# Kernel tuning notes

Hardware: AMD Instinct MI355X
Metric: run time of the kernel (lower is better)

Reference implementation:

```python
import jax, jax.numpy as jnp
import numpy as np

B, T, TREF, NBINS, H = 4096, 8192, 8192, 50, 32  # np.linspace(lo,hi,50) -> 49 bins
EPS = 1e-10


def setup_inputs() -> dict:
    key = jax.random.key(0)
    k0, k1, k2, k3, k4, k5 = jax.random.split(key, 6)
    return {
        "current_returns": jax.random.normal(k0, (B, T), jnp.float32) * 0.02,
        "reference_returns": jax.random.normal(k1, (TREF,), jnp.float32) * 0.02,
        "w1": jax.random.normal(k2, (H, 1), jnp.float32) * 0.5,   # Linear(1, H).weight
        "b1": jax.random.normal(k3, (H,), jnp.float32) * 0.1,
        "w2": jax.random.normal(k4, (H, H), jnp.float32) * 0.1,   # Linear(H, H).weight
        "b2": jax.random.normal(k5, (H,), jnp.float32) * 0.1,
    }


def _kl_from_hists(ref, curr, ref_min, ref_max):
    # Faithful to InformationTheory.kl_divergence with n_bins=50 (49 equal-width bins).
    nb = NBINS - 1
    lo = jnp.minimum(ref_min, curr.min())
    hi = jnp.maximum(ref_max, curr.max())
    width = (hi - lo) / nb

    def hist_density(x):
        # np.histogram(x, bins=linspace(lo,hi,50), density=True); all x in [lo,hi],
        # right edge goes to last bin (handled by clip).
        idx = jnp.clip(jnp.floor((x - lo) / width).astype(jnp.int32), 0, nb - 1)
        counts = jnp.zeros(nb, jnp.float32).at[idx].add(1.0)
        return counts / (x.shape[0] * width)

    p = hist_density(ref) + EPS
    q = hist_density(curr) + EPS
    p = p / p.sum()
    q = q / q.sum()
    return jnp.sum(p * jnp.log(p / q))


def reference(current_returns, reference_returns, w1, b1, w2, b2):
    ref = reference_returns
    ref_min, ref_max = ref.min(), ref.max()
    kl = jax.vmap(lambda c: _kl_from_hists(ref, c, ref_min, ref_max))(current_returns)  # [B]
    kl = jax.lax.stop_gradient(kl)  # original detaches before building kl_tensor
    x = kl[:, None]                                  # [B, 1]
    h = jax.nn.relu(x @ w1.T + b1)                   # [B, H]
    encoded = h @ w2.T + b2                          # [B, H]
    return kl, encoded
```

## Files before the change

kernel.cpp:

```cpp
#include <hip/hip_runtime.h>
#include <math.h>

constexpr int T_LEN  = 8192;
constexpr int B_ROWS = 4096;
constexpr int NB     = 49;
constexpr int NC     = 32;
constexpr int HDIM   = 32;
constexpr int FBINS  = 8192;
constexpr int ROWS   = 4;
constexpr float EPSF = 1e-10f;

constexpr int WS_CDF_OFF    = 8;
constexpr int WS_BINNED_OFF = 8208;

#define HP(i) ((i) + ((i) >> 5))

__device__ __forceinline__ void sync_lds() {
    asm volatile("s_waitcnt lgkmcnt(0)" ::: "memory");
    __builtin_amdgcn_s_barrier();
    __builtin_amdgcn_sched_barrier(0);
}

__global__ __launch_bounds__(256)
void ref_cdf_kernel(const float* __restrict__ ref, float* __restrict__ wsf) {
    __shared__ float sv[FBINS];
    __shared__ int   hist[HP(FBINS)];
    __shared__ int   wsum[4];
    __shared__ float rmn4[4], rmx4[4];
    const int tid  = threadIdx.x;
    const int lane = tid & 63;
    const int wave = tid >> 6;

    const float4* r4 = (const float4*)ref;
    float4* sv4 = (float4*)sv;
    float mn = 3.0e38f, mx = -3.0e38f;
    #pragma unroll
    for (int i = 0; i < 8; ++i) {
        float4 v = r4[tid + i * 256];
        sv4[tid + i * 256] = v;
        mn = fminf(mn, fminf(fminf(v.x, v.y), fminf(v.z, v.w)));
        mx = fmaxf(mx, fmaxf(fmaxf(v.x, v.y), fmaxf(v.z, v.w)));
    }
    for (int i = tid; i < HP(FBINS); i += 256) hist[i] = 0;
    #pragma unroll
    for (int off = 32; off > 0; off >>= 1) {
        mn = fminf(mn, __shfl_xor(mn, off));
        mx = fmaxf(mx, __shfl_xor(mx, off));
    }
    if (lane == 0) { rmn4[wave] = mn; rmx4[wave] = mx; }
    __syncthreads();
    const float rmin = fminf(fminf(rmn4[0], rmn4[1]), fminf(rmn4[2], rmn4[3]));
    const float rmax = fmaxf(fmaxf(rmx4[0], rmx4[1]), fmaxf(rmx4[2], rmx4[3]));
    const float finv = (float)FBINS / (rmax - rmin);

    for (int i = tid; i < FBINS; i += 256) {
        int fb = min(max((int)((sv[i] - rmin) * finv), 0), FBINS - 1);
        atomicAdd(&hist[HP(fb)], 1);
    }
    __syncthreads();

    const int base = tid * 32;
    int s = 0;
    #pragma unroll
    for (int j = 0; j < 32; ++j) {
        int h = hist[HP(base + j)]; hist[HP(base + j)] = s; s += h;
    }
    const int own = s;
    int incl = s;
    #pragma unroll
    for (int off = 1; off < 64; off <<= 1) {
        int t = __shfl_up(incl, off);
        if (lane >= off) incl += t;
    }
    if (lane == 63) wsum[wave] = incl;
    __syncthreads();
    int woff = 0;
    #pragma unroll
    for (int w = 0; w < 4; ++w) if (w < wave) woff += wsum[w];
    const int add = woff + incl - own;
    #pragma unroll
    for (int j = 0; j < 32; ++j) hist[HP(base + j)] += add;
    __syncthreads();

    int* cdf = (int*)(wsf + WS_CDF_OFF);
    for (int i = tid; i < FBINS; i += 256) cdf[i] = hist[HP(i)];
    if (tid == 0) { cdf[FBINS] = T_LEN; wsf[0] = rmin; wsf[1] = rmax; }
    __syncthreads();

    float* binned = wsf + WS_BINNED_OFF;
    for (int i = tid; i < FBINS; i += 256) {
        float x = sv[i];
        int fb = min(max((int)((x - rmin) * finv), 0), FBINS - 1);
        int pos = atomicAdd(&hist[HP(fb)], 1);
        binned[pos] = x;
    }
}

__global__ __launch_bounds__(256)
void kl_main_kernel(const float* __restrict__ cur,
                    const float* __restrict__ wsf,
                    const float* __restrict__ w1,
                    const float* __restrict__ b1,
                    const float* __restrict__ w2,
                    const float* __restrict__ b2,
                    float* __restrict__ kl_out,
                    float* __restrict__ enc_out) {
    __shared__ unsigned hq[NC * NB];
    __shared__ float rmnS[4], rmxS[4];
    __shared__ unsigned hrow[ROWS][NB];
    __shared__ float metaLo[ROWS], metaW[ROWS];

    const int tid  = threadIdx.x;
    const int lane = tid & 63;
    const int wave = tid >> 6;
    const int rbase = blockIdx.x * ROWS;
    const float4* src = (const float4*)(cur + (size_t)rbase * T_LEN);

    for (int i = tid; i < NC * NB; i += 256) hq[i] = 0u;
    const float rmin = wsf[0], rmax = wsf[1];

    float4 va[8], vb[8];
    #pragma unroll
    for (int i = 0; i < 8; ++i) va[i] = src[tid + i * 256];

#define ROW_STEP(V, VN, R, PF)                                                 \
    {                                                                          \
        if (PF) {                                                              \
            const float4* s2 = src + ((R) + 1) * (T_LEN / 4);                  \
            _Pragma("unroll")                                                  \
            for (int i = 0; i < 8; ++i) VN[i] = s2[tid + i * 256];             \
        }                                                                      \
        float mn = 3.0e38f, mx = -3.0e38f;                                     \
        _Pragma("unroll")                                                      \
        for (int i = 0; i < 8; ++i) {                                          \
            mn = fminf(mn, fminf(fminf(V[i].x, V[i].y), fminf(V[i].z, V[i].w)));\
            mx = fmaxf(mx, fmaxf(fmaxf(V[i].x, V[i].y), fmaxf(V[i].z, V[i].w)));\
        }                                                                      \
        _Pragma("unroll")                                                      \
        for (int off = 32; off > 0; off >>= 1) {                               \
            mn = fminf(mn, __shfl_xor(mn, off));                               \
            mx = fmaxf(mx, __shfl_xor(mx, off));                               \
        }                                                                      \
        if (lane == 0) { rmnS[wave] = mn; rmxS[wave] = mx; }                   \
        sync_lds();                                                            \
        const float lo = fminf(rmin,                                           \
            fminf(fminf(rmnS[0], rmnS[1]), fminf(rmnS[2], rmnS[3])));          \
        const float hi = fmaxf(rmax,                                           \
            fmaxf(fmaxf(rmxS[0], rmxS[1]), fmaxf(rmxS[2], rmxS[3])));          \
        const float width = (hi - lo) / (float)NB;                             \
        const float winv = 1.0f / width, nlw = -lo * winv;                     \
        unsigned* myq = hq + (tid & (NC - 1)) * NB;                            \
        _Pragma("unroll")                                                      \
        for (int i = 0; i < 8; ++i) {                                          \
            int i0 = min(max((int)fmaf(V[i].x, winv, nlw), 0), NB - 1);        \
            int i1 = min(max((int)fmaf(V[i].y, winv, nlw), 0), NB - 1);        \
            int i2 = min(max((int)fmaf(V[i].z, winv, nlw), 0), NB - 1);        \
            int i3 = min(max((int)fmaf(V[i].w, winv, nlw), 0), NB - 1);        \
            atomicAdd(&myq[i0], 1u); atomicAdd(&myq[i1], 1u);                  \
            atomicAdd(&myq[i2], 1u); atomicAdd(&myq[i3], 1u);                  \
        }                                                                      \
        sync_lds();                                                            \
        if (tid < 64 && lane < NB) {                                           \
            unsigned sq = 0;                                                   \
            _Pragma("unroll")                                                  \
            for (int c = 0; c < NC; ++c) sq += hq[c * NB + lane];              \
            hrow[R][lane] = sq;                                                \
        }                                                                      \
        if (tid == 0) { metaLo[R] = lo; metaW[R] = width; }                    \
        sync_lds();                                                            \
        for (int i = tid; i < NC * NB; i += 256) hq[i] = 0u;                   \
    }

    ROW_STEP(va, vb, 0, true)
    ROW_STEP(vb, va, 1, true)
    ROW_STEP(va, vb, 2, true)
    ROW_STEP(vb, va, 3, false)
#undef ROW_STEP

    const int row = rbase + wave;
    const float lo = metaLo[wave], width = metaW[wave];
    const bool act = lane < NB;
    const float inv = 1.0f / ((float)T_LEN * width);
    float p = 0.0f, q = 0.0f;
    if (act) q = (float)hrow[wave][lane] * inv + EPSF;

    int C = T_LEN;
    if (lane < NB - 1) {
        const float kp1  = (float)(lane + 1);
        const float finv = (float)FBINS / (rmax - rmin);
        const int* cdf = (const int*)(wsf + WS_CDF_OFF);
        const float* binned = wsf + WS_BINNED_OFF;
        const float t = fmaf(width, kp1, lo);
        int fb = (int)floorf((t - rmin) * finv);
        int a  = min(max(fb - 2, 0), FBINS);
        int bb = min(max(fb + 3, 0), FBINS);
        int ia = cdf[a], ib = cdf[bb];
        C = ia;
        for (int i = ia; i < ib; i += 4) {
            float x0 = binned[i];
            float x1 = (i + 1 < ib) ? binned[i + 1] : 3.0e38f;
            float x2 = (i + 2 < ib) ? binned[i + 2] : 3.0e38f;
            float x3 = (i + 3 < ib) ? binned[i + 3] : 3.0e38f;
            C += ((x0 - lo) / width < kp1) ? 1 : 0;
            C += ((x1 - lo) / width < kp1) ? 1 : 0;
            C += ((x2 - lo) / width < kp1) ? 1 : 0;
            C += ((x3 - lo) / width < kp1) ? 1 : 0;
        }
    }
    int Cprev = __shfl_up(C, 1);
    if (lane == 0) Cprev = 0;
    if (act) p = (float)(C - Cprev) * inv + EPSF;

    float P = p, Q = q;
    #pragma unroll
    for (int off = 32; off > 0; off >>= 1) {
        P += __shfl_xor(P, off);
        Q += __shfl_xor(Q, off);
    }
    float term = 0.0f;
    if (act) {
        const float pn = p / P;
        const float qn = q / Q;
        term = pn * logf(pn / qn);
    }
    #pragma unroll
    for (int off = 32; off > 0; off >>= 1) term += __shfl_xor(term, off);
    if (lane == 0) kl_out[row] = term;

    if (lane < HDIM) {
        float acc = b2[lane];
        #pragma unroll
        for (int t2 = 0; t2 < HDIM; ++t2) {
            float h = fmaxf(fmaf(term, w1[t2], b1[t2]), 0.0f);
            acc = fmaf(h, w2[lane * HDIM + t2], acc);
        }
        enc_out[(size_t)row * HDIM + lane] = acc;
    }
}

extern "C" void kernel_launch(void* const* d_in, const int* in_sizes, int n_in,
                              void* d_out, int out_size, void* d_ws, size_t ws_size,
                              hipStream_t stream) {
    const float* cur = (const float*)d_in[0];
    const float* ref = (const float*)d_in[1];
    const float* w1  = (const float*)d_in[2];
    const float* b1  = (const float*)d_in[3];
    const float* w2  = (const float*)d_in[4];
    const float* b2  = (const float*)d_in[5];
    float* out = (float*)d_out;
    float* wsf = (float*)d_ws;

    ref_cdf_kernel<<<1, 256, 0, stream>>>(ref, wsf);
    kl_main_kernel<<<B_ROWS / ROWS, 256, 0, stream>>>(
        cur, wsf, w1, b1, w2, b2, out, out + B_ROWS);
}
```

Baseline: 44.50 us.

## Split per-row min/max into separate kernel and bin one row per block

```diff
diff --git a/kernel.cpp b/kernel.cpp
--- a/kernel.cpp
+++ b/kernel.cpp
@@ -7,11 +7,11 @@
 constexpr int NC     = 32;
 constexpr int HDIM   = 32;
 constexpr int FBINS  = 8192;
-constexpr int ROWS   = 4;
 constexpr float EPSF = 1e-10f;
 
 constexpr int WS_CDF_OFF    = 8;
 constexpr int WS_BINNED_OFF = 8208;
+constexpr int WS_MM_OFF     = 16400;
 
 #define HP(i) ((i) + ((i) >> 5))
 
@@ -97,144 +97,140 @@
 }
 
 __global__ __launch_bounds__(256)
-void kl_main_kernel(const float* __restrict__ cur,
-                    const float* __restrict__ wsf,
-                    const float* __restrict__ w1,
-                    const float* __restrict__ b1,
-                    const float* __restrict__ w2,
-                    const float* __restrict__ b2,
-                    float* __restrict__ kl_out,
-                    float* __restrict__ enc_out) {
+void minmax_kernel(const float* __restrict__ cur, float2* __restrict__ mm) {
+    const int lane = threadIdx.x & 63;
+    const int wave = threadIdx.x >> 6;
+    const int row  = blockIdx.x * 4 + wave;
+    const float4* src = (const float4*)(cur + (size_t)row * T_LEN);
+    float mn = 3.0e38f, mx = -3.0e38f;
+    float4 c[16];
+    #pragma unroll
+    for (int i = 0; i < 16; ++i) c[i] = src[lane + i * 64];
+    #pragma unroll
+    for (int i = 0; i < 16; ++i) {
+        mn = fminf(mn, fminf(fminf(c[i].x, c[i].y), fminf(c[i].z, c[i].w)));
+        mx = fmaxf(mx, fmaxf(fmaxf(c[i].x, c[i].y), fmaxf(c[i].z, c[i].w)));
+    }
+    #pragma unroll
+    for (int i = 0; i < 16; ++i) c[i] = src[lane + (16 + i) * 64];
+    #pragma unroll
+    for (int i = 0; i < 16; ++i) {
+        mn = fminf(mn, fminf(fminf(c[i].x, c[i].y), fminf(c[i].z, c[i].w)));
+        mx = fmaxf(mx, fmaxf(fmaxf(c[i].x, c[i].y), fmaxf(c[i].z, c[i].w)));
+    }
+    #pragma unroll
+    for (int off = 32; off > 0; off >>= 1) {
+        mn = fminf(mn, __shfl_xor(mn, off));
+        mx = fmaxf(mx, __shfl_xor(mx, off));
+    }
+    if (lane == 0) mm[row] = make_float2(mn, mx);
+}
+
+__global__ __launch_bounds__(256)
+void bin_kernel(const float* __restrict__ cur,
+                const float* __restrict__ wsf,
+                const float2* __restrict__ mm,
+                const float* __restrict__ w1,
+                const float* __restrict__ b1,
+                const float* __restrict__ w2,
+                const float* __restrict__ b2,
+                float* __restrict__ kl_out,
+                float* __restrict__ enc_out) {
     __shared__ unsigned hq[NC * NB];
-    __shared__ float rmnS[4], rmxS[4];
-    __shared__ unsigned hrow[ROWS][NB];
-    __shared__ float metaLo[ROWS], metaW[ROWS];
-
+
+    const int b    = blockIdx.x;
     const int tid  = threadIdx.x;
     const int lane = tid & 63;
-    const int wave = tid >> 6;
-    const int rbase = blockIdx.x * ROWS;
-    const float4* src = (const float4*)(cur + (size_t)rbase * T_LEN);
+
+    const float4* src = (const float4*)(cur + (size_t)b * T_LEN);
+    float4 v[8];
+    #pragma unroll
+    for (int i = 0; i < 8; ++i) v[i] = src[tid + i * 256];
 
     for (int i = tid; i < NC * NB; i += 256) hq[i] = 0u;
+
     const float rmin = wsf[0], rmax = wsf[1];
-
-    float4 va[8], vb[8];
-    #pragma unroll
-    for (int i = 0; i < 8; ++i) va[i] = src[tid + i * 256];
-
-#define ROW_STEP(V, VN, R, PF)                                                 \
-    {                                                                          \
-        if (PF) {                                                              \
-            const float4* s2 = src + ((R) + 1) * (T_LEN / 4);                  \
-            _Pragma("unroll")                                                  \
-            for (int i = 0; i < 8; ++i) VN[i] = s2[tid + i * 256];             \
-        }                                                                      \
-        float mn = 3.0e38f, mx = -3.0e38f;                                     \
-        _Pragma("unroll")                                                      \
-        for (int i = 0; i < 8; ++i) {                                          \
-            mn = fminf(mn, fminf(fminf(V[i].x, V[i].y), fminf(V[i].z, V[i].w)));\
-            mx = fmaxf(mx, fmaxf(fmaxf(V[i].x, V[i].y), fmaxf(V[i].z, V[i].w)));\
-        }                                                                      \
-        _Pragma("unroll")                                                      \
-        for (int off = 32; off > 0; off >>= 1) {                               \
-            mn = fminf(mn, __shfl_xor(mn, off));                               \
-            mx = fmaxf(mx, __shfl_xor(mx, off));                               \
-        }                                                                      \
-        if (lane == 0) { rmnS[wave] = mn; rmxS[wave] = mx; }                   \
-        sync_lds();                                                            \
-        const float lo = fminf(rmin,                                           \
-            fminf(fminf(rmnS[0], rmnS[1]), fminf(rmnS[2], rmnS[3])));          \
-        const float hi = fmaxf(rmax,                                           \
-            fmaxf(fmaxf(rmxS[0], rmxS[1]), fmaxf(rmxS[2], rmxS[3])));          \
-        const float width = (hi - lo) / (float)NB;                             \
-        const float winv = 1.0f / width, nlw = -lo * winv;                     \
-        unsigned* myq = hq + (tid & (NC - 1)) * NB;                            \
-        _Pragma("unroll")                                                      \
-        for (int i = 0; i < 8; ++i) {                                          \
-            int i0 = min(max((int)fmaf(V[i].x, winv, nlw), 0), NB - 1);        \
-            int i1 = min(max((int)fmaf(V[i].y, winv, nlw), 0), NB - 1);        \
-            int i2 = min(max((int)fmaf(V[i].z, winv, nlw), 0), NB - 1);        \
-            int i3 = min(max((int)fmaf(V[i].w, winv, nlw), 0), NB - 1);        \
-            atomicAdd(&myq[i0], 1u); atomicAdd(&myq[i1], 1u);                  \
-            atomicAdd(&myq[i2], 1u); atomicAdd(&myq[i3], 1u);                  \
-        }                                                                      \
-        sync_lds();                                                            \
-        if (tid < 64 && lane < NB) {                                           \
-            unsigned sq = 0;                                                   \
-            _Pragma("unroll")                                                  \
-            for (int c = 0; c < NC; ++c) sq += hq[c * NB + lane];              \
-            hrow[R][lane] = sq;                                                \
-        }                                                                      \
-        if (tid == 0) { metaLo[R] = lo; metaW[R] = width; }                    \
-        sync_lds();                                                            \
-        for (int i = tid; i < NC * NB; i += 256) hq[i] = 0u;                   \
-    }
-
-    ROW_STEP(va, vb, 0, true)
-    ROW_STEP(vb, va, 1, true)
-    ROW_STEP(va, vb, 2, true)
-    ROW_STEP(vb, va, 3, false)
-#undef ROW_STEP
-
-    const int row = rbase + wave;
-    const float lo = metaLo[wave], width = metaW[wave];
-    const bool act = lane < NB;
-    const float inv = 1.0f / ((float)T_LEN * width);
-    float p = 0.0f, q = 0.0f;
-    if (act) q = (float)hrow[wave][lane] * inv + EPSF;
-
-    int C = T_LEN;
-    if (lane < NB - 1) {
-        const float kp1  = (float)(lane + 1);
-        const float finv = (float)FBINS / (rmax - rmin);
-        const int* cdf = (const int*)(wsf + WS_CDF_OFF);
-        const float* binned = wsf + WS_BINNED_OFF;
-        const float t = fmaf(width, kp1, lo);
-        int fb = (int)floorf((t - rmin) * finv);
-        int a  = min(max(fb - 2, 0), FBINS);
-        int bb = min(max(fb + 3, 0), FBINS);
-        int ia = cdf[a], ib = cdf[bb];
-        C = ia;
-        for (int i = ia; i < ib; i += 4) {
-            float x0 = binned[i];
-            float x1 = (i + 1 < ib) ? binned[i + 1] : 3.0e38f;
-            float x2 = (i + 2 < ib) ? binned[i + 2] : 3.0e38f;
-            float x3 = (i + 3 < ib) ? binned[i + 3] : 3.0e38f;
-            C += ((x0 - lo) / width < kp1) ? 1 : 0;
-            C += ((x1 - lo) / width < kp1) ? 1 : 0;
-            C += ((x2 - lo) / width < kp1) ? 1 : 0;
-            C += ((x3 - lo) / width < kp1) ? 1 : 0;
-        }
-    }
-    int Cprev = __shfl_up(C, 1);
-    if (lane == 0) Cprev = 0;
-    if (act) p = (float)(C - Cprev) * inv + EPSF;
-
-    float P = p, Q = q;
-    #pragma unroll
-    for (int off = 32; off > 0; off >>= 1) {
-        P += __shfl_xor(P, off);
-        Q += __shfl_xor(Q, off);
-    }
-    float term = 0.0f;
-    if (act) {
-        const float pn = p / P;
-        const float qn = q / Q;
-        term = pn * logf(pn / qn);
-    }
-    #pragma unroll
-    for (int off = 32; off > 0; off >>= 1) term += __shfl_xor(term, off);
-    if (lane == 0) kl_out[row] = term;
-
-    if (lane < HDIM) {
-        float acc = b2[lane];
+    const float2 cmm = mm[b];
+    const float lo = fminf(rmin, cmm.x);
+    const float hi = fmaxf(rmax, cmm.y);
+    const float width = (hi - lo) / (float)NB;
+    sync_lds();
+
+    const float winv = 1.0f / width, nlw = -lo * winv;
+    unsigned* myq = hq + (tid & (NC - 1)) * NB;
+    #pragma unroll
+    for (int i = 0; i < 8; ++i) {
+        int i0 = min(max((int)fmaf(v[i].x, winv, nlw), 0), NB - 1);
+        int i1 = min(max((int)fmaf(v[i].y, winv, nlw), 0), NB - 1);
+        int i2 = min(max((int)fmaf(v[i].z, winv, nlw), 0), NB - 1);
+        int i3 = min(max((int)fmaf(v[i].w, winv, nlw), 0), NB - 1);
+        atomicAdd(&myq[i0], 1u); atomicAdd(&myq[i1], 1u);
+        atomicAdd(&myq[i2], 1u); atomicAdd(&myq[i3], 1u);
+    }
+    sync_lds();
+
+    if (tid < 64) {
+        const bool act = lane < NB;
+        const float inv = 1.0f / ((float)T_LEN * width);
+        float p = 0.0f, q = 0.0f;
+        if (act) {
+            unsigned sq = 0u;
+            #pragma unroll
+            for (int c = 0; c < NC; ++c) sq += hq[c * NB + lane];
+            q = (float)sq * inv + EPSF;
+        }
+        int C = T_LEN;
+        if (lane < NB - 1) {
+            const float kp1  = (float)(lane + 1);
+            const float finv = (float)FBINS / (rmax - rmin);
+            const int* cdf = (const int*)(wsf + WS_CDF_OFF);
+            const float* binned = wsf + WS_BINNED_OFF;
+            const float t = fmaf(width, kp1, lo);
+            int fb = (int)floorf((t - rmin) * finv);
+            int a  = min(max(fb - 2, 0), FBINS);
+            int bb = min(max(fb + 3, 0), FBINS);
+            int ia = cdf[a], ib = cdf[bb];
+            C = ia;
+            for (int i = ia; i < ib; i += 4) {
+                float x0 = binned[i];
+                float x1 = (i + 1 < ib) ? binned[i + 1] : 3.0e38f;
+                float x2 = (i + 2 < ib) ? binned[i + 2] : 3.0e38f;
+                float x3 = (i + 3 < ib) ? binned[i + 3] : 3.0e38f;
+                C += ((x0 - lo) / width < kp1) ? 1 : 0;
+                C += ((x1 - lo) / width < kp1) ? 1 : 0;
+                C += ((x2 - lo) / width < kp1) ? 1 : 0;
+                C += ((x3 - lo) / width < kp1) ? 1 : 0;
+            }
+        }
+        int Cprev = __shfl_up(C, 1);
+        if (lane == 0) Cprev = 0;
+        if (act) p = (float)(C - Cprev) * inv + EPSF;
+
+        float P = p, Q = q;
         #pragma unroll
-        for (int t2 = 0; t2 < HDIM; ++t2) {
-            float h = fmaxf(fmaf(term, w1[t2], b1[t2]), 0.0f);
-            acc = fmaf(h, w2[lane * HDIM + t2], acc);
-        }
-        enc_out[(size_t)row * HDIM + lane] = acc;
+        for (int off = 32; off > 0; off >>= 1) {
+            P += __shfl_xor(P, off);
+            Q += __shfl_xor(Q, off);
+        }
+        float term = 0.0f;
+        if (act) {
+            const float pn = p / P;
+            const float qn = q / Q;
+            term = pn * logf(pn / qn);
+        }
+        #pragma unroll
+        for (int off = 32; off > 0; off >>= 1) term += __shfl_xor(term, off);
+        if (lane == 0) kl_out[b] = term;
+
+        if (lane < HDIM) {
+            float acc = b2[lane];
+            #pragma unroll
+            for (int t2 = 0; t2 < HDIM; ++t2) {
+                float h = fmaxf(fmaf(term, w1[t2], b1[t2]), 0.0f);
+                acc = fmaf(h, w2[lane * HDIM + t2], acc);
+            }
+            enc_out[(size_t)b * HDIM + lane] = acc;
+        }
     }
 }
 
@@ -249,8 +245,10 @@
     const float* b2  = (const float*)d_in[5];
     float* out = (float*)d_out;
     float* wsf = (float*)d_ws;
+    float2* mm = (float2*)(wsf + WS_MM_OFF);
 
     ref_cdf_kernel<<<1, 256, 0, stream>>>(ref, wsf);
-    kl_main_kernel<<<B_ROWS / ROWS, 256, 0, stream>>>(
-        cur, wsf, w1, b1, w2, b2, out, out + B_ROWS);
-}
+    minmax_kernel<<<B_ROWS / 4, 256, 0, stream>>>(cur, mm);
+    bin_kernel<<<B_ROWS, 256, 0, stream>>>(
+        cur, wsf, mm, w1, b1, w2, b2, out, out + B_ROWS);
+}
```

Result: slower. 60.05 us (+34.9%).
